# Performance work log

Measured on AMD Instinct MI355X. Metric: run time of the kernel, lower is better.

Reference implementation:

```python
import jax, jax.numpy as jnp
import numpy as np
from jax import lax

STRIDE = (1, 1)
PADDING = (1, 1)


def setup_inputs() -> dict:
    key = jax.random.key(0)
    k1, k2 = jax.random.split(key)
    x = jax.random.normal(k1, (32, 128, 56, 56), dtype=jnp.float32)
    kernels = jax.random.normal(k2, (256, 128, 3, 3), dtype=jnp.float32)
    return {"x": x, "kernels": kernels}


def reference(x, kernels):
    # Equivalent to the python-loop correlation conv: NCHW input, OIHW weight,
    # cross-correlation (no kernel flip), stride/padding per module config.
    out = lax.conv_general_dilated(
        x, kernels,
        window_strides=STRIDE,
        padding=[(PADDING[0], PADDING[0]), (PADDING[1], PADDING[1])],
        dimension_numbers=("NCHW", "OIHW", "NCHW"),
    )
    return out
```

## Files before the change

kernel.cpp:

```cpp
#include <hip/hip_runtime.h>
#include <cstdint>

#define N_IMG 32
#define C_IN 128
#define H_IN 56
#define W_IN 56
#define K_OUT 256
#define HW (H_IN * W_IN)
#define M_TOTAL (N_IMG * HW)
#define XP_H 58
#define XP_W 58
#define XP_ELEMS (N_IMG * XP_H * XP_W * C_IN)
#define WT_ELEMS (9 * K_OUT * C_IN)
#define NKT 36
#define BM 224
#define PATCH_PIX (6 * XP_W)
#define PATCH_SHORTS (PATCH_PIX * C_IN)
#define PATCH_UNITS (PATCH_SHORTS / 8)

typedef __bf16 bf16x8 __attribute__((ext_vector_type(8)));
typedef float f32x4 __attribute__((ext_vector_type(4)));

__device__ __align__(16) unsigned short g_xp[XP_ELEMS];
__device__ __align__(16) unsigned short g_wt[WT_ELEMS];

static __device__ __forceinline__ unsigned short f2bf(float f) {
    unsigned int u = __builtin_bit_cast(unsigned int, f);
    u += 0x7fffu + ((u >> 16) & 1u);
    return (unsigned short)(u >> 16);
}

static __device__ __forceinline__ void async_copy16(const unsigned short* g, unsigned short* l) {
    auto gp = (const __attribute__((address_space(1))) unsigned int*)g;
    auto lp = (__attribute__((address_space(3))) unsigned int*)l;
    __builtin_amdgcn_global_load_lds(gp, lp, 16, 0, 0);
}

__global__ __launch_bounds__(256) void xpose_x(const float* __restrict__ x) {
    __shared__ float tile[C_IN * 57];
    const int h = blockIdx.x;
    const int n = blockIdx.y;
    const int tid = threadIdx.x;

    if (tid < 32) {
        int col = (tid >> 4) * (XP_W - 1);
        int q = tid & 15;
        uint4* dst = (uint4*)(g_xp + ((size_t)(n * XP_H + h + 1) * XP_W + col) * C_IN) + q;
        *dst = uint4{0u, 0u, 0u, 0u};
    }
    if (h == 0 || h == H_IN - 1) {
        int hp = (h == 0) ? 0 : XP_H - 1;
        uint4* base = (uint4*)(g_xp + ((size_t)(n * XP_H + hp) * XP_W) * C_IN);
        for (int q = tid; q < (XP_W * C_IN) / 8; q += 256) base[q] = uint4{0u, 0u, 0u, 0u};
    }

#pragma unroll
    for (int i = 0; i < 28; i++) {
        int e = i * 256 + tid;
        int c = e / 56;
        int w = e - c * 56;
        tile[c * 57 + w] = x[((n * C_IN + c) * H_IN + h) * W_IN + w];
    }
    __syncthreads();
    unsigned int* outp = (unsigned int*)g_xp;
#pragma unroll
    for (int i = 0; i < 14; i++) {
        int u = i * 256 + tid;
        int w = u >> 6;
        int cp = u & 63;
        float a = tile[(2 * cp) * 57 + w];
        float b = tile[(2 * cp + 1) * 57 + w];
        unsigned int pk = (unsigned int)f2bf(a) | ((unsigned int)f2bf(b) << 16);
        int idx = ((n * XP_H + h + 1) * XP_W + (w + 1)) * C_IN + 2 * cp;
        outp[idx >> 1] = pk;
    }
}

__global__ __launch_bounds__(256) void xpose_w(const float* __restrict__ w) {
    int e = blockIdx.x * 256 + threadIdx.x;
    int rr = e >> 15;
    int rem = e & 32767;
    int k = rem >> 7;
    int c = rem & 127;
    g_wt[e] = f2bf(w[(k * C_IN + c) * 9 + rr]);
}

__global__ __launch_bounds__(512, 2) void conv_main(float* __restrict__ out) {
    __shared__ __align__(16) unsigned short patch[PATCH_SHORTS];
    __shared__ __align__(16) unsigned short Bs[4 * 8192];
    const unsigned short* __restrict__ xp = g_xp;
    const unsigned short* __restrict__ wt = g_wt;

    const int tid = threadIdx.x;
    const int wave = tid >> 6, lane = tid & 63;
    const int lr = lane & 15, lq = lane >> 4;
    const int wm0 = (wave & 1) * 112;
    const int wn0 = (wave >> 1) * 64;

    const int bid = blockIdx.x;
    const int gq = (bid & 7) * 56 + (bid >> 3);
    const int m0 = gq * 224;
    const int n_img = gq / 14;
    const int hb = (gq - n_img * 14) * 4;

    int qb[7];
#pragma unroll
    for (int mi = 0; mi < 7; mi++) {
        int pp = wm0 + mi * 16 + lr;
        qb[mi] = (pp / 56 + 1) * XP_W + (pp % 56 + 1);
    }

    const int brow = tid >> 2, bsl = tid & 3;
    const int b_srco  = brow * C_IN + ((bsl ^ ((brow >> 1) & 3)) * 8);
    const int b_srco2 = (128 + brow) * C_IN + ((bsl ^ (((128 + brow) >> 1) & 3)) * 8);
    const int b_ldso = wave * 64 * 8;

    auto stage_B = [&](int kt) {
        const unsigned short* src = wt + (kt >> 2) * (K_OUT * C_IN) + (kt & 3) * 32;
        unsigned short* dst = &Bs[(kt & 3) * 8192];
        async_copy16(src + b_srco,  dst + b_ldso);
        async_copy16(src + b_srco2, dst + 4096 + b_ldso);
    };

    const int bswz = (lq ^ ((lr >> 1) & 3)) * 8;

    const size_t srcx = (size_t)(n_img * XP_H + hb) * XP_W * C_IN;
#pragma unroll
    for (int i = 0; i < 11; i++) {
        if (i < 10 || wave < 7) {
            int u = i * 512 + tid;
            int ppix = u >> 4, sl = u & 15;
            async_copy16(xp + srcx + ppix * C_IN + ((sl ^ (ppix & 7)) * 8),
                         &patch[(i * 512 + wave * 64) * 8]);
        }
    }
    stage_B(0); stage_B(1); stage_B(2);
    asm volatile("s_waitcnt vmcnt(4)" ::: "memory");
    __builtin_amdgcn_s_barrier();
    asm volatile("" ::: "memory");

    f32x4 acc[7][4];
#pragma unroll
    for (int mi = 0; mi < 7; mi++)
#pragma unroll
        for (int nf = 0; nf < 4; nf++) acc[mi][nf] = f32x4{0.f, 0.f, 0.f, 0.f};

    for (int t = 0; t < NKT; ++t) {
        if (t + 3 < NKT) stage_B(t + 3);

        const int rs = t >> 2;
        const int r = (rs * 11) >> 5;
        const int s = rs - r * 3;
        const int dq = r * XP_W + s - (XP_W + 1);
        const int so = (t & 3) * 4 + lq;

        bf16x8 bfv[4];
#pragma unroll
        for (int nf = 0; nf < 4; nf++)
            bfv[nf] = *(const bf16x8*)(&Bs[(t & 3) * 8192 + (wn0 + nf * 16 + lr) * 32 + bswz]);
        bf16x8 af[7];
#pragma unroll
        for (int mi = 0; mi < 7; mi++) {
            int qq = qb[mi] + dq;
            af[mi] = *(const bf16x8*)(&patch[qq * C_IN + ((so ^ (qq & 7)) * 8)]);
        }
#pragma unroll
        for (int mi = 0; mi < 7; mi++)
#pragma unroll
            for (int nf = 0; nf < 4; nf++)
                acc[mi][nf] = __builtin_amdgcn_mfma_f32_16x16x32_bf16(
                    af[mi], bfv[nf], acc[mi][nf], 0, 0, 0);

        if (t < NKT - 3) {
            asm volatile("s_waitcnt vmcnt(4)" ::: "memory");
        } else if (t == NKT - 3) {
            asm volatile("s_waitcnt vmcnt(2)" ::: "memory");
        } else {
            asm volatile("s_waitcnt vmcnt(0)" ::: "memory");
        }
        __builtin_amdgcn_s_barrier();
        asm volatile("" ::: "memory");
    }

    const int off0 = m0 - n_img * HW;
#pragma unroll
    for (int mi = 0; mi < 7; mi++) {
        int off = off0 + wm0 + mi * 16 + lq * 4;
#pragma unroll
        for (int nf = 0; nf < 4; nf++) {
            int k = wn0 + nf * 16 + lr;
            *(f32x4*)(out + ((size_t)(n_img * K_OUT + k)) * HW + off) = acc[mi][nf];
        }
    }
}

extern "C" void kernel_launch(void* const* d_in, const int* in_sizes, int n_in,
                              void* d_out, int out_size, void* d_ws, size_t ws_size,
                              hipStream_t stream) {
    const float* x = (const float*)d_in[0];
    const float* w = (const float*)d_in[1];
    float* out = (float*)d_out;

    hipLaunchKernelGGL(xpose_x, dim3(H_IN, N_IMG), dim3(256), 0, stream, x);
    hipLaunchKernelGGL(xpose_w, dim3(WT_ELEMS / 256), dim3(256), 0, stream, w);
    hipLaunchKernelGGL(conv_main, dim3(M_TOTAL / BM), dim3(512), 0, stream, out);
}
```

Baseline: 227.9 us.

## Fuse input NCHW-to-NHWC bf16 transpose into conv kernel prologue

Result: faster. 213.1 us (-6.5%).

```diff
diff --git a/kernel.cpp b/kernel.cpp
--- a/kernel.cpp
+++ b/kernel.cpp
@@ -8,21 +8,16 @@
 #define K_OUT 256
 #define HW (H_IN * W_IN)
 #define M_TOTAL (N_IMG * HW)
-#define XP_H 58
 #define XP_W 58
-#define XP_ELEMS (N_IMG * XP_H * XP_W * C_IN)
 #define WT_ELEMS (9 * K_OUT * C_IN)
 #define NKT 36
 #define BM 224
 #define PATCH_PIX (6 * XP_W)
 #define PATCH_SHORTS (PATCH_PIX * C_IN)
-#define PATCH_UNITS (PATCH_SHORTS / 8)
 
 typedef __bf16 bf16x8 __attribute__((ext_vector_type(8)));
 typedef float f32x4 __attribute__((ext_vector_type(4)));
 
-__device__ __align__(16) unsigned short g_xp[XP_ELEMS];
-__device__ __align__(16) unsigned short g_wt[WT_ELEMS];
 
 static __device__ __forceinline__ unsigned short f2bf(float f) {
     unsigned int u = __builtin_bit_cast(unsigned int, f);
@@ -36,60 +31,21 @@
     __builtin_amdgcn_global_load_lds(gp, lp, 16, 0, 0);
 }
 
-__global__ __launch_bounds__(256) void xpose_x(const float* __restrict__ x) {
-    __shared__ float tile[C_IN * 57];
-    const int h = blockIdx.x;
-    const int n = blockIdx.y;
-    const int tid = threadIdx.x;
-
-    if (tid < 32) {
-        int col = (tid >> 4) * (XP_W - 1);
-        int q = tid & 15;
-        uint4* dst = (uint4*)(g_xp + ((size_t)(n * XP_H + h + 1) * XP_W + col) * C_IN) + q;
-        *dst = uint4{0u, 0u, 0u, 0u};
-    }
-    if (h == 0 || h == H_IN - 1) {
-        int hp = (h == 0) ? 0 : XP_H - 1;
-        uint4* base = (uint4*)(g_xp + ((size_t)(n * XP_H + hp) * XP_W) * C_IN);
-        for (int q = tid; q < (XP_W * C_IN) / 8; q += 256) base[q] = uint4{0u, 0u, 0u, 0u};
-    }
-
-#pragma unroll
-    for (int i = 0; i < 28; i++) {
-        int e = i * 256 + tid;
-        int c = e / 56;
-        int w = e - c * 56;
-        tile[c * 57 + w] = x[((n * C_IN + c) * H_IN + h) * W_IN + w];
-    }
-    __syncthreads();
-    unsigned int* outp = (unsigned int*)g_xp;
-#pragma unroll
-    for (int i = 0; i < 14; i++) {
-        int u = i * 256 + tid;
-        int w = u >> 6;
-        int cp = u & 63;
-        float a = tile[(2 * cp) * 57 + w];
-        float b = tile[(2 * cp + 1) * 57 + w];
-        unsigned int pk = (unsigned int)f2bf(a) | ((unsigned int)f2bf(b) << 16);
-        int idx = ((n * XP_H + h + 1) * XP_W + (w + 1)) * C_IN + 2 * cp;
-        outp[idx >> 1] = pk;
-    }
-}
-
-__global__ __launch_bounds__(256) void xpose_w(const float* __restrict__ w) {
+__global__ __launch_bounds__(256) void xpose_w(const float* __restrict__ w,
+                                               unsigned short* __restrict__ wt) {
     int e = blockIdx.x * 256 + threadIdx.x;
     int rr = e >> 15;
     int rem = e & 32767;
     int k = rem >> 7;
     int c = rem & 127;
-    g_wt[e] = f2bf(w[(k * C_IN + c) * 9 + rr]);
-}
-
-__global__ __launch_bounds__(512, 2) void conv_main(float* __restrict__ out) {
+    wt[e] = f2bf(w[(k * C_IN + c) * 9 + rr]);
+}
+
+__global__ __launch_bounds__(512, 2) void conv_main(float* __restrict__ out,
+                                                    const float* __restrict__ x,
+                                                    const unsigned short* __restrict__ wt) {
     __shared__ __align__(16) unsigned short patch[PATCH_SHORTS];
     __shared__ __align__(16) unsigned short Bs[4 * 8192];
-    const unsigned short* __restrict__ xp = g_xp;
-    const unsigned short* __restrict__ wt = g_wt;
 
     const int tid = threadIdx.x;
     const int wave = tid >> 6, lane = tid & 63;
@@ -124,20 +80,63 @@
 
     const int bswz = (lq ^ ((lr >> 1) & 3)) * 8;
 
-    const size_t srcx = (size_t)(n_img * XP_H + hb) * XP_W * C_IN;
-#pragma unroll
-    for (int i = 0; i < 11; i++) {
-        if (i < 10 || wave < 7) {
+    {
+#pragma unroll
+        for (int i = 0; i < 11; i++) {
             int u = i * 512 + tid;
-            int ppix = u >> 4, sl = u & 15;
-            async_copy16(xp + srcx + ppix * C_IN + ((sl ^ (ppix & 7)) * 8),
-                         &patch[(i * 512 + wave * 64) * 8]);
-        }
-    }
-    stage_B(0); stage_B(1); stage_B(2);
-    asm volatile("s_waitcnt vmcnt(4)" ::: "memory");
-    __builtin_amdgcn_s_barrier();
-    asm volatile("" ::: "memory");
+            if (u < PATCH_SHORTS / 8)
+                *(uint4*)&patch[u * 8] = uint4{0u, 0u, 0u, 0u};
+        }
+        stage_B(0); stage_B(1);
+
+        float* scratch = (float*)&Bs[16384];
+        const float* __restrict__ xb = x + (size_t)n_img * C_IN * HW;
+        for (int hr = 0; hr < 6; hr++) {
+            const int h = hb - 1 + hr;
+            __builtin_amdgcn_s_barrier();
+            asm volatile("" ::: "memory");
+            if (h >= 0 && h < H_IN) {
+                float v[14];
+#pragma unroll
+                for (int r = 0; r < 14; r++) {
+                    int e = r * 512 + tid;
+                    int c = e / 56, w = e - c * 56;
+                    v[r] = xb[(c * H_IN + h) * W_IN + w];
+                }
+#pragma unroll
+                for (int r = 0; r < 14; r++) {
+                    int e = r * 512 + tid;
+                    int c = e / 56, w = e - c * 56;
+                    scratch[c * 57 + w] = v[r];
+                }
+                __builtin_amdgcn_s_barrier();
+                asm volatile("" ::: "memory");
+#pragma unroll
+                for (int rr2 = 0; rr2 < 2; rr2++) {
+                    int v2 = rr2 * 512 + tid;
+                    if (v2 < 896) {
+                        int w = v2 >> 4, o = v2 & 15;
+                        unsigned int pk[4];
+#pragma unroll
+                        for (int j = 0; j < 4; j++) {
+                            float a = scratch[(o * 8 + 2 * j) * 57 + w];
+                            float b = scratch[(o * 8 + 2 * j + 1) * 57 + w];
+                            pk[j] = (unsigned int)f2bf(a) | ((unsigned int)f2bf(b) << 16);
+                        }
+                        int q = hr * XP_W + w + 1;
+                        *(uint4*)&patch[q * C_IN + ((o ^ (q & 7)) * 8)] =
+                            uint4{pk[0], pk[1], pk[2], pk[3]};
+                    }
+                }
+            }
+        }
+        __builtin_amdgcn_s_barrier();
+        asm volatile("" ::: "memory");
+        stage_B(2);
+        asm volatile("s_waitcnt vmcnt(4)" ::: "memory");
+        __builtin_amdgcn_s_barrier();
+        asm volatile("" ::: "memory");
+    }
 
     f32x4 acc[7][4];
 #pragma unroll
@@ -201,7 +200,8 @@
     const float* w = (const float*)d_in[1];
     float* out = (float*)d_out;
 
-    hipLaunchKernelGGL(xpose_x, dim3(H_IN, N_IMG), dim3(256), 0, stream, x);
-    hipLaunchKernelGGL(xpose_w, dim3(WT_ELEMS / 256), dim3(256), 0, stream, w);
-    hipLaunchKernelGGL(conv_main, dim3(M_TOTAL / BM), dim3(512), 0, stream, out);
-}
+    unsigned short* wt_ws = (unsigned short*)d_ws;
+
+    hipLaunchKernelGGL(xpose_w, dim3(WT_ELEMS / 256), dim3(256), 0, stream, w, wt_ws);
+    hipLaunchKernelGGL(conv_main, dim3(M_TOTAL / BM), dim3(512), 0, stream, out, x, wt_ws);
+}
```
